# Performance work log

Measured on AMD Instinct MI355X. Metric: run time of the kernel, lower is better.

## Reference

```python
import jax, jax.numpy as jnp
import numpy as np

VOCAB = 50000
WORD_EMB = 300
N_QNODE = 3
N_KNODE = 3
HID = 512
N_OUT = 300
N_ANS = 32000
N_LAYERS = 3
MIN_NORM = 1e-15
EPS = 1e-7

# ---- Hyperboloid manifold ops (HGCN convention, curvature c, K = 1/c) ----

def proj_tan0(u):
    # zero out the time coordinate
    return u.at[..., :1].set(0.0)

def expmap0(u, c):
    K = 1.0 / c
    sqrtK = jnp.sqrt(K)
    d = u[..., 1:]
    n = jnp.clip(jnp.linalg.norm(d, axis=-1, keepdims=True), MIN_NORM, None)
    theta = n / sqrtK
    return jnp.concatenate([sqrtK * jnp.cosh(theta), sqrtK * jnp.sinh(theta) * d / n], axis=-1)

def logmap0(x, c):
    K = 1.0 / c
    sqrtK = jnp.sqrt(K)
    d = x[..., 1:]
    n = jnp.clip(jnp.linalg.norm(d, axis=-1, keepdims=True), MIN_NORM, None)
    theta = jnp.clip(x[..., :1] / sqrtK, 1.0 + EPS, None)
    rest = sqrtK * jnp.arccosh(theta) * d / n
    return jnp.concatenate([jnp.zeros_like(rest[..., :1]), rest], axis=-1)

def proj(x, c):
    K = 1.0 / c
    d = x[..., 1:]
    first = jnp.sqrt(jnp.clip(K + jnp.sum(d * d, axis=-1, keepdims=True), EPS, None))
    return jnp.concatenate([first, d], axis=-1)

def hyperbolic_emb(x, c):
    return proj(expmap0(proj_tan0(x), c), c)


def setup_inputs() -> dict:
    key = jax.random.key(0)
    ks = jax.random.split(key, 16)
    B, NQ, NK = 256, 30, 100
    inp = {}
    inp['he_ques_id'] = jax.random.randint(ks[0], (B, NQ, N_QNODE), 0, VOCAB)
    inp['he_kg_id'] = jax.random.randint(ks[1], (B, NK, N_KNODE), 0, VOCAB)
    inp['emb_table'] = jax.random.normal(ks[2], (VOCAB, WORD_EMB), jnp.float32)
    inp['q2h_w'] = jax.random.normal(ks[3], (WORD_EMB * N_QNODE, HID), jnp.float32) * 0.01
    inp['q2h_b'] = jnp.zeros((HID,), jnp.float32)
    inp['k2h_w'] = jax.random.normal(ks[4], (WORD_EMB * N_KNODE, HID), jnp.float32) * 0.01
    inp['k2h_b'] = jnp.zeros((HID,), jnp.float32)
    inp['Wk'] = jax.random.normal(ks[5], (N_LAYERS, HID, HID), jnp.float32) * 0.05
    inp['Wq'] = jax.random.normal(ks[6], (N_LAYERS, HID, HID), jnp.float32) * 0.05
    inp['curv'] = jnp.ones((N_LAYERS + 1,), jnp.float32)
    inp['proj1_w'] = jax.random.normal(ks[7], (2 * HID, HID), jnp.float32) * 0.02
    inp['proj1_b'] = jnp.zeros((HID,), jnp.float32)
    inp['proj2_w'] = jax.random.normal(ks[8], (HID, N_OUT), jnp.float32) * 0.02
    inp['proj2_b'] = jnp.zeros((N_OUT,), jnp.float32)
    inp['glove_cands'] = jax.random.normal(ks[9], (N_ANS, N_OUT), jnp.float32)
    return inp


def reference(he_ques_id, he_kg_id, emb_table, q2h_w, q2h_b, k2h_w, k2h_b,
              Wk, Wq, curv, proj1_w, proj1_b, proj2_w, proj2_b, glove_cands):
    B = he_ques_id.shape[0]
    c0 = curv[0]
    cL = curv[N_LAYERS]

    # embedding lookup + flatten hyperedge nodes
    he_q = emb_table[he_ques_id].reshape(B, he_ques_id.shape[1], -1)  # (B,Nq,900)
    he_k = emb_table[he_kg_id].reshape(B, he_kg_id.shape[1], -1)      # (B,Nk,900)
    he_q = jnp.where(jnp.isnan(he_q), 0.0, he_q)
    he_k = jnp.where(jnp.isnan(he_k), 0.0, he_k)

    he_q = he_q @ q2h_w + q2h_b   # (B,Nq,H)
    he_k = he_k @ k2h_w + k2h_b   # (B,Nk,H)

    q = hyperbolic_emb(he_q, c0)  # (B,Nq,H) on hyperboloid
    k = hyperbolic_emb(he_k, c0)  # (B,Nk,H)

    scale = 1.0 / np.sqrt(HID)
    for i in range(N_LAYERS):
        c_in, c_out = curv[i], curv[i + 1]
        kt = proj_tan0(logmap0(k, c_in))
        qt = proj_tan0(logmap0(q, c_in))
        kp = kt @ Wk[i]
        qp = qt @ Wq[i]
        s = jnp.einsum('bkh,bqh->bkq', kp, qp) * scale
        att_k = jnp.einsum('bkq,bqh->bkh', jax.nn.softmax(s, axis=-1), qt) + kt
        att_q = jnp.einsum('bqk,bkh->bqh', jax.nn.softmax(jnp.swapaxes(s, 1, 2), axis=-1), kt) + qt
        k = proj(expmap0(proj_tan0(att_k), c_out), c_out)
        q = proj(expmap0(proj_tan0(att_q), c_out), c_out)

    # mean pool over hyperedges, concat kg||ques
    last_kq = jnp.concatenate([k.mean(axis=1), q.mean(axis=1)], axis=1)  # (B,2H)
    euc = proj_tan0(logmap0(last_kq, cL))
    h = jax.nn.relu(euc @ proj1_w + proj1_b)
    out = h @ proj2_w + proj2_b               # (B,300)
    sim = out @ glove_cands.T                 # (B,32000)
    pred = jax.nn.log_softmax(sim, axis=1)
    return pred
```

## Files before the change

kernel.cpp:

```cpp
#include <hip/hip_runtime.h>
#include <math.h>

#define BATCH 256
#define NQ 30
#define NK 100
#define HID 512
#define WORD 300
#define KIN 900
#define KP 928
#define NANS 32000
#define NOUT 300
#define NOUTP 384
#define NLAYERS 3
#define MQT (BATCH * NQ)
#define MKT (BATCH * NK)
#define SCALE 0.044194173824159216f
#define KTLD 520

typedef __attribute__((ext_vector_type(8))) short bf16x8;
typedef __attribute__((ext_vector_type(4))) float f32x4;
typedef unsigned short ushort_t;

__device__ __forceinline__ unsigned short f2bf(float f) {
  unsigned int u = __float_as_uint(f);
  u = (u + 0x7FFF + ((u >> 16) & 1)) >> 16;
  return (unsigned short)u;
}
__device__ __forceinline__ float bf2f(unsigned short s) {
  return __uint_as_float(((unsigned int)s) << 16);
}

typedef const __attribute__((address_space(1))) unsigned int* gas_u32;
typedef __attribute__((address_space(3))) unsigned int* las_u32;
__device__ __forceinline__ void gld_lds16(const void* g, void* l) {
  __builtin_amdgcn_global_load_lds((gas_u32)g, (las_u32)l, 16, 0, 0);
}

__device__ __forceinline__ int xcd_swz_linear() {
  const int nwg = gridDim.x * gridDim.y;
  const int orig = blockIdx.y * gridDim.x + blockIdx.x;
  const int q = nwg >> 3, r = nwg & 7;
  const int xcd = orig & 7, idx = orig >> 3;
  return (xcd < r ? xcd * (q + 1) : r * (q + 1) + (xcd - r) * q) + idx;
}

__device__ __forceinline__ float waveReduceSum(float v) {
#pragma unroll
  for (int o = 32; o > 0; o >>= 1) v += __shfl_xor(v, o);
  return v;
}
__device__ float blockReduceSum512(float v) {
  __shared__ float sm[8];
  int lane = threadIdx.x & 63, w = threadIdx.x >> 6;
  v = waveReduceSum(v);
  if (lane == 0) sm[w] = v;
  __syncthreads();
  float r = 0.f;
#pragma unroll
  for (int i = 0; i < 8; ++i) r += sm[i];
  __syncthreads();
  return r;
}

__device__ __forceinline__ bf16x8 castrow8(const float* __restrict__ rowp, int kb) {
  union { ushort_t u[8]; bf16x8 v; } pk;
  if (kb + 8 <= NOUT) {
    float2 a0 = *(const float2*)(rowp + kb);
    float2 a1 = *(const float2*)(rowp + kb + 2);
    float2 a2 = *(const float2*)(rowp + kb + 4);
    float2 a3 = *(const float2*)(rowp + kb + 6);
    pk.u[0] = f2bf(a0.x); pk.u[1] = f2bf(a0.y);
    pk.u[2] = f2bf(a1.x); pk.u[3] = f2bf(a1.y);
    pk.u[4] = f2bf(a2.x); pk.u[5] = f2bf(a2.y);
    pk.u[6] = f2bf(a3.x); pk.u[7] = f2bf(a3.y);
  } else {
#pragma unroll
    for (int j = 0; j < 8; ++j) {
      const int kk = kb + j;
      pk.u[j] = (kk < NOUT) ? f2bf(rowp[kk]) : (ushort_t)0;
    }
  }
  return pk.v;
}

template <int BF32B, int BIAS, int OUTF32, int OUTBF16, int ZC0, int RELU>
__global__ __launch_bounds__(256) void mfma_gemm2(
    const ushort_t* __restrict__ A1, const ushort_t* __restrict__ Bt1,
    const float* __restrict__ bias1, float* __restrict__ C1,
    ushort_t* __restrict__ Cb1, int M1b,
    const ushort_t* __restrict__ A2, const ushort_t* __restrict__ Bt2,
    const float* __restrict__ bias2, float* __restrict__ C2,
    ushort_t* __restrict__ Cb2, const float* __restrict__ Bf,
    size_t zsA, size_t zsB, size_t zsC,
    int N, int K, int nbias) {
  __shared__ __align__(16) ushort_t Abuf[2][128 * 32];
  __shared__ __align__(16) ushort_t Bbuf[2][128 * 32];
  const int wg = xcd_swz_linear();
  const int bx = wg % gridDim.x, by = wg / gridDim.x;
  const int z = blockIdx.z;
  const bool sel = (by >= M1b);
  const ushort_t* A = (sel ? A2 : A1) + z * zsA;
  const ushort_t* Bt = (sel ? Bt2 : Bt1) + z * zsB;
  const float* bias = sel ? bias2 : bias1;
  float* C = (sel ? C2 : C1);
  ushort_t* Cb = (sel ? Cb2 : Cb1);
  if (C) C += z * zsC;
  if (Cb) Cb += z * zsC;
  const int row0 = (sel ? (by - M1b) : by) * 128;
  const int col0 = bx * 128;

  const int tid = threadIdx.x;
  const int lane = tid & 63, w = tid >> 6;
  const int wr = w >> 1, wc = w & 1;
  const int s_r = lane & 15, s_kq = lane >> 4;

  const size_t a_src0 = (size_t)(row0 + (w * 2 + 0) * 16 + s_r) * K + s_kq * 8;
  const size_t a_src1 = (size_t)(row0 + (w * 2 + 1) * 16 + s_r) * K + s_kq * 8;
  const size_t b_src0 = (size_t)(col0 + (w * 2 + 0) * 16 + s_r) * K + s_kq * 8;
  const size_t b_src1 = (size_t)(col0 + (w * 2 + 1) * 16 + s_r) * K + s_kq * 8;
  const float* bf_row0 = BF32B ? (Bf + (size_t)(col0 + (w * 2 + 0) * 16 + s_r) * NOUT) : nullptr;
  const float* bf_row1 = BF32B ? (Bf + (size_t)(col0 + (w * 2 + 1) * 16 + s_r) * NOUT) : nullptr;

  auto stageAB = [&](int t, int bsel) {
    const int k0 = t * 32;
    gld_lds16(A + a_src0 + k0, Abuf[bsel] + (w * 2 + 0) * 512);
    gld_lds16(A + a_src1 + k0, Abuf[bsel] + (w * 2 + 1) * 512);
    if (BF32B) {
      const int kb = k0 + s_kq * 8;
      *(bf16x8*)(Bbuf[bsel] + (w * 2 + 0) * 512 + lane * 8) = castrow8(bf_row0, kb);
      *(bf16x8*)(Bbuf[bsel] + (w * 2 + 1) * 512 + lane * 8) = castrow8(bf_row1, kb);
    } else {
      gld_lds16(Bt + b_src0 + k0, Bbuf[bsel] + (w * 2 + 0) * 512);
      gld_lds16(Bt + b_src1 + k0, Bbuf[bsel] + (w * 2 + 1) * 512);
    }
  };

  f32x4 acc[4][4];
#pragma unroll
  for (int i = 0; i < 4; ++i)
#pragma unroll
    for (int j = 0; j < 4; ++j) acc[i][j] = (f32x4){0.f, 0.f, 0.f, 0.f};

  const int nt = K / 32;
  stageAB(0, 0);
  __syncthreads();
  for (int t = 0; t < nt; ++t) {
    const int cur = t & 1;
    if (t + 1 < nt) stageAB(t + 1, cur ^ 1);
    bf16x8 af[4], bfr[4];
#pragma unroll
    for (int mi = 0; mi < 4; ++mi)
      af[mi] = *(const bf16x8*)(Abuf[cur] + (wr * 4 + mi) * 512 + lane * 8);
#pragma unroll
    for (int nj = 0; nj < 4; ++nj)
      bfr[nj] = *(const bf16x8*)(Bbuf[cur] + (wc * 4 + nj) * 512 + lane * 8);
#pragma unroll
    for (int mi = 0; mi < 4; ++mi)
#pragma unroll
      for (int nj = 0; nj < 4; ++nj)
        acc[mi][nj] = __builtin_amdgcn_mfma_f32_16x16x32_bf16(
            af[mi], bfr[nj], acc[mi][nj], 0, 0, 0);
    __syncthreads();
  }

#pragma unroll
  for (int nj = 0; nj < 4; ++nj) {
    const int n = col0 + wc * 64 + nj * 16 + (lane & 15);
    const float bb = BIAS ? ((n < nbias) ? bias[n] : 0.f) : 0.f;
#pragma unroll
    for (int mi = 0; mi < 4; ++mi) {
      f32x4 v = acc[mi][nj];
#pragma unroll
      for (int r = 0; r < 4; ++r) {
        const int m = row0 + wr * 64 + mi * 16 + (lane >> 4) * 4 + r;
        float val = v[r] + bb;
        if (RELU) val = fmaxf(val, 0.f);
        if (ZC0 && n == 0) val = 0.f;
        if (OUTF32) C[(size_t)m * N + n] = val;
        if (OUTBF16) Cb[(size_t)m * N + n] = f2bf(val);
      }
    }
  }
}

__global__ __launch_bounds__(256) void gather_all_k(
    const int* __restrict__ qid, const int* __restrict__ kid,
    const float* __restrict__ emb, ushort_t* __restrict__ gq,
    ushort_t* __restrict__ gk) {
  int m = blockIdx.x;
  const int* ids;
  ushort_t* outp;
  if (m < MQT) {
    ids = qid + m * 3;
    outp = gq + (size_t)m * KP;
  } else {
    m -= MQT;
    ids = kid + m * 3;
    outp = gk + (size_t)m * KP;
  }
  const int t = threadIdx.x;
  if (t >= KP / 4) return;
  const int k = t * 4;
  ushort4 o = make_ushort4(0, 0, 0, 0);
  if (k < KIN) {
    const int node = (k >= 600) ? 2 : ((k >= 300) ? 1 : 0);
    const int off = k - node * 300;
    const int id = ids[node];
    float4 v = *(const float4*)(emb + (size_t)id * 300 + off);
    if (v.x != v.x) v.x = 0.f;
    if (v.y != v.y) v.y = 0.f;
    if (v.z != v.z) v.z = 0.f;
    if (v.w != v.w) v.w = 0.f;
    o = make_ushort4(f2bf(v.x), f2bf(v.y), f2bf(v.z), f2bf(v.w));
  }
  *(ushort4*)(outp + k) = o;
}

__global__ __launch_bounds__(256) void tcast4_k(
    const float* __restrict__ q2h_w, const float* __restrict__ k2h_w,
    const float* __restrict__ p1w, const float* __restrict__ p2w,
    ushort_t* __restrict__ q2h_wt, ushort_t* __restrict__ k2h_wt,
    ushort_t* __restrict__ p1wt, ushort_t* __restrict__ p2wt) {
  const int z = blockIdx.z;
  const float* src;
  ushort_t* dst;
  int R, Cc, Rp, Cp;
  if (z == 0)      { src = q2h_w; dst = q2h_wt; R = KIN;  Cc = HID;  Rp = KP;   Cp = HID; }
  else if (z == 1) { src = k2h_w; dst = k2h_wt; R = KIN;  Cc = HID;  Rp = KP;   Cp = HID; }
  else if (z == 2) { src = p1w; dst = p1wt; R = 1024; Cc = HID;  Rp = 1024; Cp = HID; }
  else             { src = p2w; dst = p2wt; R = HID;  Cc = NOUT; Rp = HID;  Cp = NOUTP; }
  const int r0 = blockIdx.y * 32, c0 = blockIdx.x * 32;
  if (r0 >= Rp || c0 >= Cp) return;
  __shared__ float t[32][33];
  const int tx = threadIdx.x & 31, ty = threadIdx.x >> 5;
#pragma unroll
  for (int i = 0; i < 4; ++i) {
    int r = r0 + ty + i * 8, c = c0 + tx;
    t[ty + i * 8][tx] = (r < R && c < Cc) ? src[(size_t)r * Cc + c] : 0.f;
  }
  __syncthreads();
#pragma unroll
  for (int i = 0; i < 4; ++i) {
    int c = c0 + ty + i * 8, r = r0 + tx;
    if (c < Cp && r < Rp) dst[(size_t)c * Rp + r] = f2bf(t[tx][ty + i * 8]);
  }
}

__global__ __launch_bounds__(128) void castrows_k(
    const float* __restrict__ Wk, const float* __restrict__ Wq,
    ushort_t* __restrict__ Wkr, ushort_t* __restrict__ Wqr) {
  const int idx = blockIdx.x;
  const int mat = idx >> 9, row = idx & 511;
  const float* src = (mat < 3 ? Wk + (size_t)mat * HID * HID
                              : Wq + (size_t)(mat - 3) * HID * HID) + (size_t)row * HID;
  ushort_t* dst = (mat < 3 ? Wkr + (size_t)mat * HID * HID
                           : Wqr + (size_t)(mat - 3) * HID * HID) + (size_t)row * HID;
  const int k = threadIdx.x * 4;
  float4 v = *(const float4*)(src + k);
  *(ushort4*)(dst + k) = make_ushort4(f2bf(v.x), f2bf(v.y), f2bf(v.z), f2bf(v.w));
}

__global__ __launch_bounds__(512) void att_fused_k(
    const ushort_t* __restrict__ Qp, const ushort_t* __restrict__ Ktc,
    const ushort_t* __restrict__ Qc, ushort_t* __restrict__ Kn,
    ushort_t* __restrict__ Qn) {
  const int b = blockIdx.x;
  __shared__ float S_lds[NK][32];
  __shared__ float PqT[NK][32];
  __shared__ __align__(16) ushort_t kts[NK * KTLD];
  __shared__ __align__(16) ushort_t qts[NQ * HID];
  const int tid = threadIdx.x;
  const int w = tid >> 6, lane = tid & 63;
  const ushort_t* ktg = Ktc + (size_t)b * NK * HID;
  const ushort_t* qtg = Qc + (size_t)b * NQ * HID;

  for (int e = tid; e < NK * 64; e += 512) {
    const int r = e >> 6, c16 = e & 63;
    gld_lds16(ktg + (size_t)r * HID + c16 * 8, kts + (size_t)r * KTLD + c16 * 8);
  }
  for (int e = tid; e < NQ * 64; e += 512) {
    const int r = e >> 6, c16 = e & 63;
    gld_lds16(qtg + (size_t)r * HID + c16 * 8, qts + (size_t)r * HID + c16 * 8);
  }
  __syncthreads();

  if (w < 7) {
    const int r = lane & 15, kq = lane >> 4;
    const ushort_t* qpb = Qp + (size_t)b * NQ * HID;
    const int rowA = w * 16 + r;
    const int rowA_c = (rowA < NK) ? rowA : (NK - 1);
    const int qr1 = (16 + r) < NQ ? (16 + r) : NQ - 1;
    f32x4 a0 = {0.f, 0.f, 0.f, 0.f}, a1 = {0.f, 0.f, 0.f, 0.f};
    for (int k0 = 0; k0 < HID; k0 += 32) {
      bf16x8 af = *(const bf16x8*)(kts + (size_t)rowA_c * KTLD + k0 + kq * 8);
      bf16x8 b0 = *(const bf16x8*)(qpb + (size_t)r * HID + k0 + kq * 8);
      bf16x8 b1 = *(const bf16x8*)(qpb + (size_t)qr1 * HID + k0 + kq * 8);
      a0 = __builtin_amdgcn_mfma_f32_16x16x32_bf16(af, b0, a0, 0, 0, 0);
      a1 = __builtin_amdgcn_mfma_f32_16x16x32_bf16(af, b1, a1, 0, 0, 0);
    }
    const int q0 = lane & 15, mb = (lane >> 4) * 4;
#pragma unroll
    for (int rr = 0; rr < 4; ++rr) {
      const int mA = w * 16 + mb + rr;
      if (mA < NK) {
        S_lds[mA][q0] = a0[rr] * SCALE;
        if (q0 + 16 < NQ) S_lds[mA][q0 + 16] = a1[rr] * SCALE;
      }
    }
  }
  __syncthreads();
  if (tid < NQ) {
    const int q = tid;
    float m = -1e30f;
    for (int kr = 0; kr < NK; ++kr) m = fmaxf(m, S_lds[kr][q]);
    float s = 0.f;
    for (int kr = 0; kr < NK; ++kr) {
      float e = expf(S_lds[kr][q] - m);
      PqT[kr][q] = e;
      s += e;
    }
    float inv = 1.f / s;
    for (int kr = 0; kr < NK; ++kr) PqT[kr][q] *= inv;
  } else if (tid >= 32 && tid < 32 + NK) {
    const int kr = tid - 32;
    PqT[kr][30] = 0.f;
    PqT[kr][31] = 0.f;
  }
  __syncthreads();
  if (tid < NK) {
    const int kr = tid;
    float m = -1e30f;
#pragma unroll
    for (int q = 0; q < NQ; ++q) m = fmaxf(m, S_lds[kr][q]);
    float s = 0.f;
    float e[NQ];
#pragma unroll
    for (int q = 0; q < NQ; ++q) {
      e[q] = expf(S_lds[kr][q] - m);
      s += e[q];
    }
    float inv = 1.f / s;
#pragma unroll
    for (int q = 0; q < NQ; ++q) S_lds[kr][q] = e[q] * inv;
    S_lds[kr][30] = 0.f;
    S_lds[kr][31] = 0.f;
  }
  __syncthreads();

  const int c = tid;
  float qx[32], ax[32];
#pragma unroll
  for (int q = 0; q < NQ; ++q) qx[q] = bf2f(qts[q * HID + c]);
  qx[30] = 0.f;
  qx[31] = 0.f;
#pragma unroll
  for (int i = 0; i < 32; ++i) ax[i] = 0.f;
  ushort_t* kout = Kn + (size_t)b * NK * HID;
  for (int kr = 0; kr < NK; ++kr) {
    const float kx = bf2f(kts[(size_t)kr * KTLD + c]);
    float sx = kx;
#pragma unroll
    for (int g = 0; g < 8; ++g) {
      float4 pk = *(const float4*)&S_lds[kr][g * 4];
      sx = fmaf(pk.x, qx[g * 4 + 0], sx);
      sx = fmaf(pk.y, qx[g * 4 + 1], sx);
      sx = fmaf(pk.z, qx[g * 4 + 2], sx);
      sx = fmaf(pk.w, qx[g * 4 + 3], sx);
      float4 pq = *(const float4*)&PqT[kr][g * 4];
      ax[g * 4 + 0] = fmaf(pq.x, kx, ax[g * 4 + 0]);
      ax[g * 4 + 1] = fmaf(pq.y, kx, ax[g * 4 + 1]);
      ax[g * 4 + 2] = fmaf(pq.z, kx, ax[g * 4 + 2]);
      ax[g * 4 + 3] = fmaf(pq.w, kx, ax[g * 4 + 3]);
    }
    kout[(size_t)kr * HID + c] = f2bf(sx);
  }
  ushort_t* qout = Qn + (size_t)b * NQ * HID;
#pragma unroll
  for (int q = 0; q < NQ; ++q)
    qout[(size_t)q * HID + c] = f2bf(ax[q] + qx[q]);
}

__global__ __launch_bounds__(512) void finale_k(
    const ushort_t* __restrict__ Kb, const ushort_t* __restrict__ Qb,
    ushort_t* __restrict__ lastb, const float* __restrict__ curv) {
  const int b = blockIdx.x, tid = threadIdx.x;
  const int w = tid >> 6, lane = tid & 63;
  const float c = curv[NLAYERS];
  const float Kc = 1.f / c, sqrtK = sqrtf(Kc);
  __shared__ float fsc[NK + NQ];
  __shared__ float fst[NK + NQ];
  const ushort_t* xkp = Kb + (size_t)b * NK * HID;
  const ushort_t* xqp = Qb + (size_t)b * NQ * HID;

  for (int r = w; r < NK + NQ; r += 8) {
    const ushort_t* row =
        (r < NK) ? (xkp + (size_t)r * HID) : (xqp + (size_t)(r - NK) * HID);
    bf16x8 v = *(const bf16x8*)(row + lane * 8);
    float ss = 0.f;
#pragma unroll
    for (int j = 0; j < 8; ++j) {
      float t = bf2f((unsigned short)v[j]);
      ss = fmaf(t, t, ss);
    }
    ss = waveReduceSum(ss);
    if (lane == 0) {
      float n = fmaxf(sqrtf(ss), 1e-15f);
      float f = sqrtK * sinhf(n / sqrtK) / n;
      fsc[r] = f;
      fst[r] = sqrtf(fmaxf(Kc + f * f * ss, 1e-7f));
    }
  }
  __syncthreads();

  float mk, mq;
  if (tid == 0) {
    float sk = 0.f, sq2 = 0.f;
    for (int r = 0; r < NK; ++r) sk += fst[r];
    for (int r = 0; r < NQ; ++r) sq2 += fst[NK + r];
    mk = sk;
    mq = sq2;
  } else {
    float sk = 0.f, sq2 = 0.f;
    for (int r = 0; r < NK; ++r)
      sk = fmaf(fsc[r], bf2f(xkp[(size_t)r * HID + tid]), sk);
    for (int r = 0; r < NQ; ++r)
      sq2 = fmaf(fsc[NK + r], bf2f(xqp[(size_t)r * HID + tid]), sq2);
    mk = sk;
    mq = sq2;
  }
  mk *= (1.f / NK);
  mq *= (1.f / NQ);

  float sq = ((tid == 0) ? 0.f : mk * mk) + mq * mq;
  float ssall = blockReduceSum512(sq);
  __shared__ float x0sh;
  if (tid == 0) x0sh = mk;
  __syncthreads();
  const float x0 = x0sh;
  const float n = fmaxf(sqrtf(ssall), 1e-15f);
  const float theta = fmaxf(x0 / sqrtK, 1.f + 1e-7f);
  const float rr = sqrtK * acoshf(theta) / n;
  ushort_t* ob = lastb + (size_t)b * 1024;
  ob[tid] = (tid == 0) ? (ushort_t)0 : f2bf(rr * mk);
  ob[512 + tid] = f2bf(rr * mq);
}

__global__ __launch_bounds__(512) void logsoftmax_k(float* __restrict__ x) {
  const int b = blockIdx.x, tid = threadIdx.x;
  float4* row = (float4*)(x + (size_t)b * NANS);
  float m = -3.4e38f, s = 0.f;
  for (int i = tid; i < NANS / 4; i += 512) {
    float4 v = row[i];
    float lm = fmaxf(fmaxf(v.x, v.y), fmaxf(v.z, v.w));
    float nm = fmaxf(m, lm);
    s = s * expf(m - nm) + expf(v.x - nm) + expf(v.y - nm) +
        expf(v.z - nm) + expf(v.w - nm);
    m = nm;
  }
#pragma unroll
  for (int o = 32; o > 0; o >>= 1) {
    float mo = __shfl_xor(m, o);
    float so = __shfl_xor(s, o);
    float nm = fmaxf(m, mo);
    s = s * expf(m - nm) + so * expf(mo - nm);
    m = nm;
  }
  __shared__ float smm[8], sms[8];
  const int w = tid >> 6, lane = tid & 63;
  if (lane == 0) { smm[w] = m; sms[w] = s; }
  __syncthreads();
  float gm = smm[0], gs = sms[0];
#pragma unroll
  for (int i = 1; i < 8; ++i) {
    float nm = fmaxf(gm, smm[i]);
    gs = gs * expf(gm - nm) + sms[i] * expf(smm[i] - nm);
    gm = nm;
  }
  const float lse = gm + logf(gs);
  for (int i = tid; i < NANS / 4; i += 512) {
    float4 v = row[i];
    v.x -= lse; v.y -= lse; v.z -= lse; v.w -= lse;
    row[i] = v;
  }
}

extern "C" void kernel_launch(void* const* d_in, const int* in_sizes, int n_in,
                              void* d_out, int out_size, void* d_ws, size_t ws_size,
                              hipStream_t stream) {
  const int* qid = (const int*)d_in[0];
  const int* kid = (const int*)d_in[1];
  const float* emb = (const float*)d_in[2];
  const float* q2h_w = (const float*)d_in[3];
  const float* q2h_b = (const float*)d_in[4];
  const float* k2h_w = (const float*)d_in[5];
  const float* k2h_b = (const float*)d_in[6];
  const float* Wk = (const float*)d_in[7];
  const float* Wq = (const float*)d_in[8];
  const float* curv = (const float*)d_in[9];
  const float* p1w = (const float*)d_in[10];
  const float* p1b = (const float*)d_in[11];
  const float* p2w = (const float*)d_in[12];
  const float* p2b = (const float*)d_in[13];
  const float* glove = (const float*)d_in[14];
  float* out = (float*)d_out;

  ushort_t* u = (ushort_t*)d_ws;
  ushort_t* Ks0 = u;
  ushort_t* Ks1 = Ks0 + (size_t)MKT * HID;
  ushort_t* Qs0 = Ks1 + (size_t)MKT * HID;
  ushort_t* Qs1 = Qs0 + (size_t)MQT * HID;
  ushort_t* Qps = Qs1 + (size_t)MQT * HID;
  ushort_t* gq = Qps + (size_t)MQT * HID;
  ushort_t* gk = gq + (size_t)MQT * KP;
  ushort_t* q2h_wt = gk + (size_t)MKT * KP;
  ushort_t* k2h_wt = q2h_wt + (size_t)HID * KP;
  ushort_t* Wkr = k2h_wt + (size_t)HID * KP;
  ushort_t* Wqr = Wkr + (size_t)NLAYERS * HID * HID;
  ushort_t* Mb = Wqr + (size_t)NLAYERS * HID * HID;
  ushort_t* p1wt = Mb + (size_t)NLAYERS * HID * HID;
  ushort_t* p2wt = p1wt + (size_t)HID * 1024;
  ushort_t* lastb = p2wt + (size_t)NOUTP * HID;
  ushort_t* h1b = lastb + (size_t)BATCH * 1024;
  ushort_t* o2b = h1b + (size_t)BATCH * HID;

  gather_all_k<<<MQT + MKT, 256, 0, stream>>>(qid, kid, emb, gq, gk);
  tcast4_k<<<dim3(16, 32, 4), 256, 0, stream>>>(
      q2h_w, k2h_w, p1w, p2w, q2h_wt, k2h_wt, p1wt, p2wt);
  castrows_k<<<6 * HID, 128, 0, stream>>>(Wk, Wq, Wkr, Wqr);

  mfma_gemm2<0, 0, 0, 1, 0, 0><<<dim3(HID / 128, HID / 128, NLAYERS), 256, 0, stream>>>(
      Wkr, Wqr, nullptr, nullptr, Mb, HID / 128,
      Wkr, Wqr, nullptr, nullptr, Mb, nullptr,
      (size_t)HID * HID, (size_t)HID * HID, (size_t)HID * HID, HID, HID, HID);

  mfma_gemm2<0, 1, 0, 1, 1, 0><<<dim3(HID / 128, MQT / 128 + MKT / 128), 256, 0, stream>>>(
      gq, q2h_wt, q2h_b, nullptr, Qs0, MQT / 128,
      gk, k2h_wt, k2h_b, nullptr, Ks0, nullptr, 0, 0, 0, HID, KP, HID);

  ushort_t* Kc = Ks0;
  ushort_t* Kn = Ks1;
  ushort_t* Qc = Qs0;
  ushort_t* Qn = Qs1;
  for (int i = 0; i < NLAYERS; ++i) {
    mfma_gemm2<0, 0, 0, 1, 0, 0><<<dim3(HID / 128, MQT / 128), 256, 0, stream>>>(
        Qc, Mb + (size_t)i * HID * HID, nullptr, nullptr, Qps, MQT / 128,
        Qc, Mb + (size_t)i * HID * HID, nullptr, nullptr, Qps, nullptr,
        0, 0, 0, HID, HID, HID);
    att_fused_k<<<BATCH, 512, 0, stream>>>(Qps, Kc, Qc, Kn, Qn);
    ushort_t* t1 = Kc; Kc = Kn; Kn = t1;
    ushort_t* t2 = Qc; Qc = Qn; Qn = t2;
  }

  finale_k<<<BATCH, 512, 0, stream>>>(Kc, Qc, lastb, curv);

  mfma_gemm2<0, 1, 0, 1, 0, 1><<<dim3(HID / 128, BATCH / 128), 256, 0, stream>>>(
      lastb, p1wt, p1b, nullptr, h1b, BATCH / 128,
      lastb, p1wt, p1b, nullptr, h1b, nullptr, 0, 0, 0, HID, 1024, HID);
  mfma_gemm2<0, 1, 0, 1, 0, 0><<<dim3(NOUTP / 128, BATCH / 128), 256, 0, stream>>>(
      h1b, p2wt, p2b, nullptr, o2b, BATCH / 128,
      h1b, p2wt, p2b, nullptr, o2b, nullptr, 0, 0, 0, NOUTP, HID, NOUT);
  mfma_gemm2<1, 0, 1, 0, 0, 0><<<dim3(NANS / 128, BATCH / 128), 256, 0, stream>>>(
      o2b, nullptr, nullptr, out, nullptr, BATCH / 128,
      o2b, nullptr, nullptr, out, nullptr, glove, 0, 0, 0, NANS, NOUTP, NANS);
  logsoftmax_k<<<BATCH, 512, 0, stream>>>(out);
}
```

Before: 451.0 us.

## Pre-swizzle GEMM operands into MFMA tile-panel layout for contiguous loads

```diff
diff --git a/kernel.cpp b/kernel.cpp
--- a/kernel.cpp
+++ b/kernel.cpp
@@ -8,9 +8,11 @@
 #define WORD 300
 #define KIN 900
 #define KP 928
+#define NTIN 29
 #define NANS 32000
 #define NOUT 300
 #define NOUTP 384
+#define NTG 12
 #define NLAYERS 3
 #define MQT (BATCH * NQ)
 #define MKT (BATCH * NK)
@@ -62,35 +64,14 @@
   return r;
 }
 
-__device__ __forceinline__ bf16x8 castrow8(const float* __restrict__ rowp, int kb) {
-  union { ushort_t u[8]; bf16x8 v; } pk;
-  if (kb + 8 <= NOUT) {
-    float2 a0 = *(const float2*)(rowp + kb);
-    float2 a1 = *(const float2*)(rowp + kb + 2);
-    float2 a2 = *(const float2*)(rowp + kb + 4);
-    float2 a3 = *(const float2*)(rowp + kb + 6);
-    pk.u[0] = f2bf(a0.x); pk.u[1] = f2bf(a0.y);
-    pk.u[2] = f2bf(a1.x); pk.u[3] = f2bf(a1.y);
-    pk.u[4] = f2bf(a2.x); pk.u[5] = f2bf(a2.y);
-    pk.u[6] = f2bf(a3.x); pk.u[7] = f2bf(a3.y);
-  } else {
-#pragma unroll
-    for (int j = 0; j < 8; ++j) {
-      const int kk = kb + j;
-      pk.u[j] = (kk < NOUT) ? f2bf(rowp[kk]) : (ushort_t)0;
-    }
-  }
-  return pk.v;
-}
-
-template <int BF32B, int BIAS, int OUTF32, int OUTBF16, int ZC0, int RELU>
+template <int SWZA, int SWZB, int BIAS, int OUTF32, int OUTBF16, int ZC0, int RELU>
 __global__ __launch_bounds__(256) void mfma_gemm2(
     const ushort_t* __restrict__ A1, const ushort_t* __restrict__ Bt1,
     const float* __restrict__ bias1, float* __restrict__ C1,
     ushort_t* __restrict__ Cb1, int M1b,
     const ushort_t* __restrict__ A2, const ushort_t* __restrict__ Bt2,
     const float* __restrict__ bias2, float* __restrict__ C2,
-    ushort_t* __restrict__ Cb2, const float* __restrict__ Bf,
+    ushort_t* __restrict__ Cb2,
     size_t zsA, size_t zsB, size_t zsC,
     int N, int K, int nbias) {
   __shared__ __align__(16) ushort_t Abuf[2][128 * 32];
@@ -113,25 +94,31 @@
   const int lane = tid & 63, w = tid >> 6;
   const int wr = w >> 1, wc = w & 1;
   const int s_r = lane & 15, s_kq = lane >> 4;
-
-  const size_t a_src0 = (size_t)(row0 + (w * 2 + 0) * 16 + s_r) * K + s_kq * 8;
-  const size_t a_src1 = (size_t)(row0 + (w * 2 + 1) * 16 + s_r) * K + s_kq * 8;
-  const size_t b_src0 = (size_t)(col0 + (w * 2 + 0) * 16 + s_r) * K + s_kq * 8;
-  const size_t b_src1 = (size_t)(col0 + (w * 2 + 1) * 16 + s_r) * K + s_kq * 8;
-  const float* bf_row0 = BF32B ? (Bf + (size_t)(col0 + (w * 2 + 0) * 16 + s_r) * NOUT) : nullptr;
-  const float* bf_row1 = BF32B ? (Bf + (size_t)(col0 + (w * 2 + 1) * 16 + s_r) * NOUT) : nullptr;
+  const int nt = K / 32;
+
+  const size_t a_lin0 = (size_t)(row0 + (w * 2 + 0) * 16 + s_r) * K + s_kq * 8;
+  const size_t a_lin1 = (size_t)(row0 + (w * 2 + 1) * 16 + s_r) * K + s_kq * 8;
+  const size_t b_lin0 = (size_t)(col0 + (w * 2 + 0) * 16 + s_r) * K + s_kq * 8;
+  const size_t b_lin1 = (size_t)(col0 + (w * 2 + 1) * 16 + s_r) * K + s_kq * 8;
+  const size_t a_swz0 = ((size_t)(row0 >> 7) * nt) * 4096 + (w * 2 + 0) * 512 + lane * 8;
+  const size_t a_swz1 = a_swz0 + 512;
+  const size_t b_swz0 = ((size_t)(col0 >> 7) * nt) * 4096 + (w * 2 + 0) * 512 + lane * 8;
+  const size_t b_swz1 = b_swz0 + 512;
 
   auto stageAB = [&](int t, int bsel) {
-    const int k0 = t * 32;
-    gld_lds16(A + a_src0 + k0, Abuf[bsel] + (w * 2 + 0) * 512);
-    gld_lds16(A + a_src1 + k0, Abuf[bsel] + (w * 2 + 1) * 512);
-    if (BF32B) {
-      const int kb = k0 + s_kq * 8;
-      *(bf16x8*)(Bbuf[bsel] + (w * 2 + 0) * 512 + lane * 8) = castrow8(bf_row0, kb);
-      *(bf16x8*)(Bbuf[bsel] + (w * 2 + 1) * 512 + lane * 8) = castrow8(bf_row1, kb);
+    if (SWZA) {
+      gld_lds16(A + a_swz0 + (size_t)t * 4096, Abuf[bsel] + (w * 2 + 0) * 512);
+      gld_lds16(A + a_swz1 + (size_t)t * 4096, Abuf[bsel] + (w * 2 + 1) * 512);
     } else {
-      gld_lds16(Bt + b_src0 + k0, Bbuf[bsel] + (w * 2 + 0) * 512);
-      gld_lds16(Bt + b_src1 + k0, Bbuf[bsel] + (w * 2 + 1) * 512);
+      gld_lds16(A + a_lin0 + t * 32, Abuf[bsel] + (w * 2 + 0) * 512);
+      gld_lds16(A + a_lin1 + t * 32, Abuf[bsel] + (w * 2 + 1) * 512);
+    }
+    if (SWZB) {
+      gld_lds16(Bt + b_swz0 + (size_t)t * 4096, Bbuf[bsel] + (w * 2 + 0) * 512);
+      gld_lds16(Bt + b_swz1 + (size_t)t * 4096, Bbuf[bsel] + (w * 2 + 1) * 512);
+    } else {
+      gld_lds16(Bt + b_lin0 + t * 32, Bbuf[bsel] + (w * 2 + 0) * 512);
+      gld_lds16(Bt + b_lin1 + t * 32, Bbuf[bsel] + (w * 2 + 1) * 512);
     }
   };
 
@@ -141,7 +128,6 @@
 #pragma unroll
     for (int j = 0; j < 4; ++j) acc[i][j] = (f32x4){0.f, 0.f, 0.f, 0.f};
 
-  const int nt = K / 32;
   stageAB(0, 0);
   __syncthreads();
   for (int t = 0; t < nt; ++t) {
@@ -189,14 +175,14 @@
     ushort_t* __restrict__ gk) {
   int m = blockIdx.x;
   const int* ids;
-  ushort_t* outp;
+  ushort_t* buf;
   if (m < MQT) {
     ids = qid + m * 3;
-    outp = gq + (size_t)m * KP;
+    buf = gq;
   } else {
     m -= MQT;
     ids = kid + m * 3;
-    outp = gk + (size_t)m * KP;
+    buf = gk;
   }
   const int t = threadIdx.x;
   if (t >= KP / 4) return;
@@ -213,22 +199,76 @@
     if (v.w != v.w) v.w = 0.f;
     o = make_ushort4(f2bf(v.x), f2bf(v.y), f2bf(v.z), f2bf(v.w));
   }
-  *(ushort4*)(outp + k) = o;
-}
-
-__global__ __launch_bounds__(256) void tcast4_k(
+  const int panel = m >> 7, chunk = (m & 127) >> 4, rl = m & 15;
+  ushort_t* dst = buf + ((size_t)panel * NTIN + (k >> 5)) * 4096 +
+                  chunk * 512 + ((k >> 3) & 3) * 128 + rl * 8 + (k & 7);
+  *(ushort4*)dst = o;
+}
+
+__global__ __launch_bounds__(256) void wcast_swz_k(
     const float* __restrict__ q2h_w, const float* __restrict__ k2h_w,
+    ushort_t* __restrict__ q2s, ushort_t* __restrict__ k2s) {
+  const float* wsrc = blockIdx.z ? k2h_w : q2h_w;
+  ushort_t* dst = (blockIdx.z ? k2s : q2s) +
+                  ((size_t)blockIdx.y * NTIN + blockIdx.x) * 4096;
+  const int ts = blockIdx.x, cp = blockIdx.y;
+  for (int g = threadIdx.x; g < 512; g += 256) {
+    const int o = g * 8;
+    const int chunk = o >> 9, kq = (o >> 7) & 3, rl = (o >> 3) & 15;
+    const int col = cp * 128 + chunk * 16 + rl;
+    const int kb = ts * 32 + kq * 8;
+    ushort_t tmp[8];
+#pragma unroll
+    for (int j = 0; j < 8; ++j) {
+      const int k = kb + j;
+      tmp[j] = (k < KIN) ? f2bf(wsrc[(size_t)k * HID + col]) : (ushort_t)0;
+    }
+    *(ushort4*)(dst + o) = make_ushort4(tmp[0], tmp[1], tmp[2], tmp[3]);
+    *(ushort4*)(dst + o + 4) = make_ushort4(tmp[4], tmp[5], tmp[6], tmp[7]);
+  }
+}
+
+__global__ __launch_bounds__(256) void gcast_swz_k(
+    const float* __restrict__ glove, ushort_t* __restrict__ gs) {
+  const int ts = blockIdx.x, gp = blockIdx.y;
+  ushort_t* dst = gs + ((size_t)gp * NTG + ts) * 4096;
+  for (int g = threadIdx.x; g < 512; g += 256) {
+    const int o = g * 8;
+    const int chunk = o >> 9, kq = (o >> 7) & 3, rl = (o >> 3) & 15;
+    const int row = gp * 128 + chunk * 16 + rl;
+    const int kb = ts * 32 + kq * 8;
+    ushort_t tmp[8];
+    if (kb + 8 <= NOUT) {
+      const float* s = glove + (size_t)row * NOUT + kb;
+      float2 a0 = *(const float2*)(s + 0);
+      float2 a1 = *(const float2*)(s + 2);
+      float2 a2 = *(const float2*)(s + 4);
+      float2 a3 = *(const float2*)(s + 6);
+      tmp[0] = f2bf(a0.x); tmp[1] = f2bf(a0.y);
+      tmp[2] = f2bf(a1.x); tmp[3] = f2bf(a1.y);
+      tmp[4] = f2bf(a2.x); tmp[5] = f2bf(a2.y);
+      tmp[6] = f2bf(a3.x); tmp[7] = f2bf(a3.y);
+    } else {
+#pragma unroll
+      for (int j = 0; j < 8; ++j) {
+        const int k = kb + j;
+        tmp[j] = (k < NOUT) ? f2bf(glove[(size_t)row * NOUT + k]) : (ushort_t)0;
+      }
+    }
+    *(ushort4*)(dst + o) = make_ushort4(tmp[0], tmp[1], tmp[2], tmp[3]);
+    *(ushort4*)(dst + o + 4) = make_ushort4(tmp[4], tmp[5], tmp[6], tmp[7]);
+  }
+}
+
+__global__ __launch_bounds__(256) void tcast2_k(
     const float* __restrict__ p1w, const float* __restrict__ p2w,
-    ushort_t* __restrict__ q2h_wt, ushort_t* __restrict__ k2h_wt,
     ushort_t* __restrict__ p1wt, ushort_t* __restrict__ p2wt) {
   const int z = blockIdx.z;
   const float* src;
   ushort_t* dst;
   int R, Cc, Rp, Cp;
-  if (z == 0)      { src = q2h_w; dst = q2h_wt; R = KIN;  Cc = HID;  Rp = KP;   Cp = HID; }
-  else if (z == 1) { src = k2h_w; dst = k2h_wt; R = KIN;  Cc = HID;  Rp = KP;   Cp = HID; }
-  else if (z == 2) { src = p1w; dst = p1wt; R = 1024; Cc = HID;  Rp = 1024; Cp = HID; }
-  else             { src = p2w; dst = p2wt; R = HID;  Cc = NOUT; Rp = HID;  Cp = NOUTP; }
+  if (z == 0) { src = p1w; dst = p1wt; R = 1024; Cc = HID;  Rp = 1024; Cp = HID; }
+  else        { src = p2w; dst = p2wt; R = HID;  Cc = NOUT; Rp = HID;  Cp = NOUTP; }
   const int r0 = blockIdx.y * 32, c0 = blockIdx.x * 32;
   if (r0 >= Rp || c0 >= Cp) return;
   __shared__ float t[32][33];
@@ -511,10 +551,11 @@
   ushort_t* Qs1 = Qs0 + (size_t)MQT * HID;
   ushort_t* Qps = Qs1 + (size_t)MQT * HID;
   ushort_t* gq = Qps + (size_t)MQT * HID;
-  ushort_t* gk = gq + (size_t)MQT * KP;
-  ushort_t* q2h_wt = gk + (size_t)MKT * KP;
-  ushort_t* k2h_wt = q2h_wt + (size_t)HID * KP;
-  ushort_t* Wkr = k2h_wt + (size_t)HID * KP;
+  ushort_t* gk = gq + (size_t)(MQT / 128) * NTIN * 4096;
+  ushort_t* q2s = gk + (size_t)(MKT / 128) * NTIN * 4096;
+  ushort_t* k2s = q2s + (size_t)4 * NTIN * 4096;
+  ushort_t* gsw = k2s + (size_t)4 * NTIN * 4096;
+  ushort_t* Wkr = gsw + (size_t)250 * NTG * 4096;
   ushort_t* Wqr = Wkr + (size_t)NLAYERS * HID * HID;
   ushort_t* Mb = Wqr + (size_t)NLAYERS * HID * HID;
   ushort_t* p1wt = Mb + (size_t)NLAYERS * HID * HID;
@@ -524,27 +565,28 @@
   ushort_t* o2b = h1b + (size_t)BATCH * HID;
 
   gather_all_k<<<MQT + MKT, 256, 0, stream>>>(qid, kid, emb, gq, gk);
-  tcast4_k<<<dim3(16, 32, 4), 256, 0, stream>>>(
-      q2h_w, k2h_w, p1w, p2w, q2h_wt, k2h_wt, p1wt, p2wt);
+  wcast_swz_k<<<dim3(NTIN, 4, 2), 256, 0, stream>>>(q2h_w, k2h_w, q2s, k2s);
+  gcast_swz_k<<<dim3(NTG, 250), 256, 0, stream>>>(glove, gsw);
+  tcast2_k<<<dim3(16, 32, 2), 256, 0, stream>>>(p1w, p2w, p1wt, p2wt);
   castrows_k<<<6 * HID, 128, 0, stream>>>(Wk, Wq, Wkr, Wqr);
 
-  mfma_gemm2<0, 0, 0, 1, 0, 0><<<dim3(HID / 128, HID / 128, NLAYERS), 256, 0, stream>>>(
+  mfma_gemm2<0, 0, 0, 0, 1, 0, 0><<<dim3(HID / 128, HID / 128, NLAYERS), 256, 0, stream>>>(
       Wkr, Wqr, nullptr, nullptr, Mb, HID / 128,
-      Wkr, Wqr, nullptr, nullptr, Mb, nullptr,
+      Wkr, Wqr, nullptr, nullptr, Mb,
       (size_t)HID * HID, (size_t)HID * HID, (size_t)HID * HID, HID, HID, HID);
 
-  mfma_gemm2<0, 1, 0, 1, 1, 0><<<dim3(HID / 128, MQT / 128 + MKT / 128), 256, 0, stream>>>(
-      gq, q2h_wt, q2h_b, nullptr, Qs0, MQT / 128,
-      gk, k2h_wt, k2h_b, nullptr, Ks0, nullptr, 0, 0, 0, HID, KP, HID);
+  mfma_gemm2<1, 1, 1, 0, 1, 1, 0><<<dim3(HID / 128, MQT / 128 + MKT / 128), 256, 0, stream>>>(
+      gq, q2s, q2h_b, nullptr, Qs0, MQT / 128,
+      gk, k2s, k2h_b, nullptr, Ks0, 0, 0, 0, HID, KP, HID);
 
   ushort_t* Kc = Ks0;
   ushort_t* Kn = Ks1;
   ushort_t* Qc = Qs0;
   ushort_t* Qn = Qs1;
   for (int i = 0; i < NLAYERS; ++i) {
-    mfma_gemm2<0, 0, 0, 1, 0, 0><<<dim3(HID / 128, MQT / 128), 256, 0, stream>>>(
+    mfma_gemm2<0, 0, 0, 0, 1, 0, 0><<<dim3(HID / 128, MQT / 128), 256, 0, stream>>>(
         Qc, Mb + (size_t)i * HID * HID, nullptr, nullptr, Qps, MQT / 128,
-        Qc, Mb + (size_t)i * HID * HID, nullptr, nullptr, Qps, nullptr,
+        Qc, Mb + (size_t)i * HID * HID, nullptr, nullptr, Qps,
         0, 0, 0, HID, HID, HID);
     att_fused_k<<<BATCH, 512, 0, stream>>>(Qps, Kc, Qc, Kn, Qn);
     ushort_t* t1 = Kc; Kc = Kn; Kn = t1;
@@ -553,14 +595,14 @@
 
   finale_k<<<BATCH, 512, 0, stream>>>(Kc, Qc, lastb, curv);
 
-  mfma_gemm2<0, 1, 0, 1, 0, 1><<<dim3(HID / 128, BATCH / 128), 256, 0, stream>>>(
+  mfma_gemm2<0, 0, 1, 0, 1, 0, 1><<<dim3(HID / 128, BATCH / 128), 256, 0, stream>>>(
       lastb, p1wt, p1b, nullptr, h1b, BATCH / 128,
-      lastb, p1wt, p1b, nullptr, h1b, nullptr, 0, 0, 0, HID, 1024, HID);
-  mfma_gemm2<0, 1, 0, 1, 0, 0><<<dim3(NOUTP / 128, BATCH / 128), 256, 0, stream>>>(
+      lastb, p1wt, p1b, nullptr, h1b, 0, 0, 0, HID, 1024, HID);
+  mfma_gemm2<0, 0, 1, 0, 1, 0, 0><<<dim3(NOUTP / 128, BATCH / 128), 256, 0, stream>>>(
       h1b, p2wt, p2b, nullptr, o2b, BATCH / 128,
-      h1b, p2wt, p2b, nullptr, o2b, nullptr, 0, 0, 0, NOUTP, HID, NOUT);
-  mfma_gemm2<1, 0, 1, 0, 0, 0><<<dim3(NANS / 128, BATCH / 128), 256, 0, stream>>>(
-      o2b, nullptr, nullptr, out, nullptr, BATCH / 128,
-      o2b, nullptr, nullptr, out, nullptr, glove, 0, 0, 0, NANS, NOUTP, NANS);
+      h1b, p2wt, p2b, nullptr, o2b, 0, 0, 0, NOUTP, HID, NOUT);
+  mfma_gemm2<0, 1, 0, 1, 0, 0, 0><<<dim3(NANS / 128, BATCH / 128), 256, 0, stream>>>(
+      o2b, gsw, nullptr, out, nullptr, BATCH / 128,
+      o2b, gsw, nullptr, out, nullptr, 0, 0, 0, NANS, NOUTP, NANS);
   logsoftmax_k<<<BATCH, 512, 0, stream>>>(out);
 }
```

Measured after the change: 509.7 us. 1.13x slower.
